# Optimization experiments

Measured on AMD Instinct MI355X. Metric: run time of the kernel, lower is better.

The kernel has to match this reference:

```python
import jax, jax.numpy as jnp
import numpy as np

V, D, N, T, U, E = 200000, 128, 50000, 20, 128, 128

def setup_inputs() -> dict:
    key = jax.random.key(0)
    ks = jax.random.split(key, 12)
    s = 0.02
    return {
        "node_ids": jax.random.randint(ks[0], (N,), 0, V, dtype=jnp.int32),
        "neigh_ids": jax.random.randint(ks[1], (N, T), 0, V, dtype=jnp.int32),
        "alpha": jax.random.uniform(ks[2], (N, T), dtype=jnp.float32),
        "table": jax.random.normal(ks[3], (V, D), dtype=jnp.float32),
        "Wq": jax.random.normal(ks[4], (D, U), dtype=jnp.float32) * s,
        "bq": jnp.zeros((U,), dtype=jnp.float32),
        "Wn": jax.random.normal(ks[5], (D, U), dtype=jnp.float32) * s,
        "bn": jnp.zeros((U,), dtype=jnp.float32),
        "Ww": jax.random.normal(ks[6], (2 * U, U), dtype=jnp.float32) * s,
        "bw": jnp.zeros((U,), dtype=jnp.float32),
        "Wg": jax.random.normal(ks[7], (U, E), dtype=jnp.float32) * s,
        "bg": jnp.zeros((E,), dtype=jnp.float32),
    }

def reference(node_ids, neigh_ids, alpha, table, Wq, bq, Wn, bn, Ww, bw, Wg, bg):
    # gather initial embeddings (irregular indexing)
    node_x = table[node_ids]            # [N, D]
    neigh_x = table[neigh_ids]          # [N, T, D]
    # Convolve: node branch Dense+ReLU
    node_h = jax.nn.relu(node_x @ Wq + bq)                       # [N, U]
    # Aggregator: neighbor Dense+ReLU then alpha-weighted matmul
    neigh_h = jax.nn.relu(jnp.einsum('ntd,du->ntu', neigh_x, Wn) + bn)  # [N, T, U]
    agg = jnp.einsum('nt,ntu->nu', alpha, neigh_h)               # [N, U]
    # concat + Dense+ReLU
    emb = jax.nn.relu(jnp.concatenate([node_h, agg], axis=-1) @ Ww + bw)  # [N, U]
    # global (Frobenius) L2 normalize, as in tf.divide(Emb, tf.norm(Emb, ord=2))
    emb = emb / jnp.linalg.norm(emb)
    # final Dense+ReLU to emb_dim
    return jax.nn.relu(emb @ Wg + bg)                            # [N, E]
```

## Files before the change

kernel.cpp:

```cpp
#include <hip/hip_runtime.h>
#include <math.h>


using f32x4  = __attribute__((ext_vector_type(4))) float;
using short8 = __attribute__((ext_vector_type(8))) short;

__device__ __forceinline__ ushort f2bf(float f) {
    uint u = __float_as_uint(f);
    return (ushort)((u + 0x7fffu + ((u >> 16) & 1u)) >> 16);
}
__device__ __forceinline__ float bf2f(ushort h) {
    return __uint_as_float((uint)h << 16);
}
__device__ __forceinline__ uint pk2(float lo, float hi) {
    return (uint)f2bf(lo) | ((uint)f2bf(hi) << 16);
}
__device__ __forceinline__ short8 pack8(f32x4 a, f32x4 b) {
    uint u0 = pk2(a[0], a[1]), u1 = pk2(a[2], a[3]);
    uint u2 = pk2(b[0], b[1]), u3 = pk2(b[2], b[3]);
    uint4 r; r.x = u0; r.y = u1; r.z = u2; r.w = u3;
    union { uint4 u; short8 s; } cv; cv.u = r; return cv.s;
}

__global__ __launch_bounds__(256)
void prep_weights(const float* __restrict__ Wq, const float* __restrict__ Wn,
                  const float* __restrict__ Ww, const float* __restrict__ Wg,
                  ushort* __restrict__ WqT, ushort* __restrict__ WnT,
                  ushort* __restrict__ WwT, ushort* __restrict__ WgT)
{
    int idx = blockIdx.x * 256 + threadIdx.x;
    const float* W; ushort* WT; int K; int j = idx;
    if (j < 16384)      { W = Wq; WT = WqT; K = 128; }
    else if (j < 32768) { W = Wn; WT = WnT; K = 128; j -= 16384; }
    else if (j < 65536) { W = Ww; WT = WwT; K = 256; j -= 32768; }
    else                { W = Wg; WT = WgT; K = 128; j -= 65536; }
    int n = j & 127, k = j >> 7;
    WT[(size_t)n * K + k] = f2bf(W[j]);
}

template<int KTOT, bool GATHER, bool AFP32, bool SUMSQ, bool SCALE, bool OUTFP32>
__global__ __launch_bounds__(256, 2)
void mfma_gemm(const void* __restrict__ Av, int lda,
               const int* __restrict__ gidx,
               const ushort* __restrict__ WT,
               const float* __restrict__ bias,
               void* __restrict__ outv, int ldo, int M,
               float* __restrict__ partials,
               const float* __restrict__ scale_ptr)
{
    __shared__ __align__(16) ushort Blds[128 * 128];
    __shared__ float red[256];

    const int tid = threadIdx.x;
    const int w = tid >> 6, l = tid & 63;
    const int l16 = l & 15, lh = l >> 4;
    const int brow = blockIdx.x * 128;

    const int row0 = brow + 32 * w + l16;
    const int row1 = row0 + 16;
    int g0 = (row0 < M) ? row0 : (M - 1);
    int g1 = (row1 < M) ? row1 : (M - 1);
    if (GATHER) { g0 = gidx[g0]; g1 = gidx[g1]; }

    f32x4 acc[2][8];
#pragma unroll
    for (int nt = 0; nt < 2; ++nt)
#pragma unroll
        for (int mt = 0; mt < 8; ++mt)
#pragma unroll
            for (int i = 0; i < 4; ++i) acc[nt][mt][i] = 0.f;

    for (int kc = 0; kc < KTOT / 128; ++kc) {
        const int kbase = kc * 128;

        short8 a[2][4];
        f32x4 t[2][8];
        if (AFP32) {
            const float* A = (const float*)Av;
#pragma unroll
            for (int nt = 0; nt < 2; ++nt) {
                const float* rp = A + (size_t)(nt ? g1 : g0) * lda + kbase + 8 * lh;
#pragma unroll
                for (int ks = 0; ks < 4; ++ks) {
                    t[nt][2 * ks]     = *reinterpret_cast<const f32x4*>(rp + 32 * ks);
                    t[nt][2 * ks + 1] = *reinterpret_cast<const f32x4*>(rp + 32 * ks + 4);
                }
            }
        } else {
            const ushort* A = (const ushort*)Av;
#pragma unroll
            for (int nt = 0; nt < 2; ++nt) {
                const ushort* rp = A + (size_t)(nt ? g1 : g0) * lda + kbase + 8 * lh;
#pragma unroll
                for (int ks = 0; ks < 4; ++ks)
                    a[nt][ks] = *reinterpret_cast<const short8*>(rp + 32 * ks);
            }
        }

        if (kc > 0) __syncthreads();
#pragma unroll
        for (int it = 0; it < 8; ++it) {
            int idx = it * 256 + tid;
            int n = idx >> 4, o = idx & 15;
            uint4 v = *reinterpret_cast<const uint4*>(&WT[(size_t)n * KTOT + kbase + 8 * o]);
            *reinterpret_cast<uint4*>(
                (char*)Blds + n * 256 + ((16 * o) ^ ((n & 7) << 4))) = v;
        }
        __syncthreads();

        if (AFP32) {
#pragma unroll
            for (int nt = 0; nt < 2; ++nt)
#pragma unroll
                for (int ks = 0; ks < 4; ++ks)
                    a[nt][ks] = pack8(t[nt][2 * ks], t[nt][2 * ks + 1]);
        }

#pragma unroll
        for (int ks = 0; ks < 4; ++ks) {
#pragma unroll
            for (int mt = 0; mt < 8; ++mt) {
                short8 wf = *reinterpret_cast<const short8*>(
                    (char*)Blds + (16 * mt + l16) * 256 +
                    ((64 * ks + 16 * lh) ^ ((l16 & 7) << 4)));
                acc[0][mt] = __builtin_amdgcn_mfma_f32_16x16x32_bf16(wf, a[0][ks], acc[0][mt], 0, 0, 0);
                acc[1][mt] = __builtin_amdgcn_mfma_f32_16x16x32_bf16(wf, a[1][ks], acc[1][mt], 0, 0, 0);
            }
        }
    }

    const float scale = SCALE ? scale_ptr[0] : 1.0f;
    float ssq = 0.f;
#pragma unroll
    for (int nt = 0; nt < 2; ++nt) {
        const int row = nt ? row1 : row0;
        const bool ok = row < M;
#pragma unroll
        for (int mt = 0; mt < 8; ++mt) {
            const f32x4 bv = *reinterpret_cast<const f32x4*>(&bias[16 * mt + 4 * lh]);
            f32x4 v;
#pragma unroll
            for (int i = 0; i < 4; ++i)
                v[i] = fmaxf(fmaf(acc[nt][mt][i], scale, bv[i]), 0.f);
            if (SUMSQ && ok)
                ssq += v[0] * v[0] + v[1] * v[1] + v[2] * v[2] + v[3] * v[3];
            if (OUTFP32) {
                if (ok)
                    *reinterpret_cast<f32x4*>(
                        &((float*)outv)[(size_t)row * ldo + 16 * mt + 4 * lh]) = v;
            } else {
                uint2 p; p.x = pk2(v[0], v[1]); p.y = pk2(v[2], v[3]);
                if (ok)
                    *reinterpret_cast<uint2*>(
                        &((ushort*)outv)[(size_t)row * ldo + 16 * mt + 4 * lh]) = p;
            }
        }
    }

    if (SUMSQ) {
        red[tid] = ssq;
        __syncthreads();
        for (int st = 128; st > 0; st >>= 1) {
            if (tid < st) red[tid] += red[tid + st];
            __syncthreads();
        }
        if (tid == 0) partials[blockIdx.x] = red[0];
    }
}

__global__ __launch_bounds__(256)
void agg_bf16(const ushort* __restrict__ H,
              const int* __restrict__ nids,
              const float* __restrict__ alpha,
              ushort* __restrict__ outb,
              int N)
{
    const int n   = blockIdx.x * 16 + (threadIdx.x >> 4);
    const int l16 = threadIdx.x & 15;
    if (n >= N) return;

    const int*   idp = &nids[n * 20];
    const float* alp = &alpha[n * 20];
    float a[8];
#pragma unroll
    for (int j = 0; j < 8; ++j) a[j] = 0.f;

#pragma unroll
    for (int t = 0; t < 20; ++t) {
        const int   id = idp[t];
        const float al = alp[t];
        uint4 h = *reinterpret_cast<const uint4*>(&H[(size_t)id * 128 + 8 * l16]);
        a[0] = fmaf(al, bf2f((ushort)(h.x & 0xffff)), a[0]);
        a[1] = fmaf(al, bf2f((ushort)(h.x >> 16)),    a[1]);
        a[2] = fmaf(al, bf2f((ushort)(h.y & 0xffff)), a[2]);
        a[3] = fmaf(al, bf2f((ushort)(h.y >> 16)),    a[3]);
        a[4] = fmaf(al, bf2f((ushort)(h.z & 0xffff)), a[4]);
        a[5] = fmaf(al, bf2f((ushort)(h.z >> 16)),    a[5]);
        a[6] = fmaf(al, bf2f((ushort)(h.w & 0xffff)), a[6]);
        a[7] = fmaf(al, bf2f((ushort)(h.w >> 16)),    a[7]);
    }
    uint4 p;
    p.x = pk2(a[0], a[1]);
    p.y = pk2(a[2], a[3]);
    p.z = pk2(a[4], a[5]);
    p.w = pk2(a[6], a[7]);
    *reinterpret_cast<uint4*>(&outb[(size_t)n * 256 + 8 * l16]) = p;
}

__global__ void reduce_norm(const float* __restrict__ partials, int n,
                            float* __restrict__ scale)
{
    __shared__ float red[256];
    float s = 0.f;
    for (int i = threadIdx.x; i < n; i += 256) s += partials[i];
    red[threadIdx.x] = s;
    __syncthreads();
    for (int st = 128; st > 0; st >>= 1) {
        if (threadIdx.x < st) red[threadIdx.x] += red[threadIdx.x + st];
        __syncthreads();
    }
    if (threadIdx.x == 0) scale[0] = 1.0f / sqrtf(red[0]);
}

extern "C" void kernel_launch(void* const* d_in, const int* in_sizes, int n_in,
                              void* d_out, int out_size, void* d_ws, size_t ws_size,
                              hipStream_t stream)
{
    const int*   node_ids  = (const int*)  d_in[0];
    const int*   neigh_ids = (const int*)  d_in[1];
    const float* alpha     = (const float*)d_in[2];
    const float* table     = (const float*)d_in[3];
    const float* Wq        = (const float*)d_in[4];
    const float* bq        = (const float*)d_in[5];
    const float* Wn        = (const float*)d_in[6];
    const float* bn        = (const float*)d_in[7];
    const float* Ww        = (const float*)d_in[8];
    const float* bw        = (const float*)d_in[9];
    const float* Wg        = (const float*)d_in[10];
    const float* bg        = (const float*)d_in[11];

    const int N = in_sizes[0];
    const int V = in_sizes[3] / 128;
    float* out = (float*)d_out;

    ushort* H    = (ushort*)d_ws;
    ushort* nh   = H    + (size_t)V * 128;
    ushort* embb = nh   + (size_t)N * 256;
    ushort* WqT  = embb + (size_t)N * 128;
    ushort* WnT  = WqT  + 16384;
    ushort* WwT  = WnT  + 16384;
    ushort* WgT  = WwT  + 32768;
    float*  partials = (float*)(WgT + 16384);
    float*  scale    = partials + 512;

    const size_t need = (size_t)((char*)(scale + 16) - (char*)d_ws);
    if (ws_size < need) return;

    const int nblkN = (N + 127) / 128;
    const int nblkV = (V + 127) / 128;

    prep_weights<<<320, 256, 0, stream>>>(Wq, Wn, Ww, Wg, WqT, WnT, WwT, WgT);
    mfma_gemm<128, false, true, false, false, false><<<nblkV, 256, 0, stream>>>(
        table, 128, nullptr, WnT, bn, H, 128, V, nullptr, nullptr);
    mfma_gemm<128, true, true, false, false, false><<<nblkN, 256, 0, stream>>>(
        table, 128, node_ids, WqT, bq, nh, 256, N, nullptr, nullptr);
    agg_bf16<<<(N + 15) / 16, 256, 0, stream>>>(H, neigh_ids, alpha, nh + 128, N);
    mfma_gemm<256, false, false, true, false, false><<<nblkN, 256, 0, stream>>>(
        nh, 256, nullptr, WwT, bw, embb, 128, N, partials, nullptr);
    reduce_norm<<<1, 256, 0, stream>>>(partials, nblkN, scale);
    mfma_gemm<128, false, false, false, true, true><<<nblkN, 256, 0, stream>>>(
        embb, 128, nullptr, WgT, bg, out, 128, N, nullptr, scale);
}
```

Baseline: 125.1 us.

## Use persistent grid-stride MFMA kernels, merge node/table GEMMs, fuse norm reduction

Replaces the generic one-shot GEMM kernel with persistent grid-stride kernels that stage weights into LDS once per block and then loop over 16-row tiles. The table-wide and gathered node GEMMs are merged into one launch that splits blocks between them, and the next tile's fp32 rows are prefetched while the current tile is computed. The norm reduction is folded into the final GEMM, which removes one launch. The aim is to amortise weight staging, cut launch count and improve latency hiding. The trade-offs are a smaller per-wave tile (16 rows instead of 32), so each weight fragment read from LDS feeds half as many MFMAs, and redundant partial-sum reduction in every final block.

```diff
diff --git a/kernel.cpp b/kernel.cpp
--- a/kernel.cpp
+++ b/kernel.cpp
@@ -16,9 +16,9 @@
     return (uint)f2bf(lo) | ((uint)f2bf(hi) << 16);
 }
 __device__ __forceinline__ short8 pack8(f32x4 a, f32x4 b) {
-    uint u0 = pk2(a[0], a[1]), u1 = pk2(a[2], a[3]);
-    uint u2 = pk2(b[0], b[1]), u3 = pk2(b[2], b[3]);
-    uint4 r; r.x = u0; r.y = u1; r.z = u2; r.w = u3;
+    uint4 r;
+    r.x = pk2(a[0], a[1]); r.y = pk2(a[2], a[3]);
+    r.z = pk2(b[0], b[1]); r.w = pk2(b[2], b[3]);
     union { uint4 u; short8 s; } cv; cv.u = r; return cv.s;
 }
 
@@ -38,133 +38,109 @@
     WT[(size_t)n * K + k] = f2bf(W[j]);
 }
 
-template<int KTOT, bool GATHER, bool AFP32, bool SUMSQ, bool SCALE, bool OUTFP32>
-__global__ __launch_bounds__(256, 2)
-void mfma_gemm(const void* __restrict__ Av, int lda,
-               const int* __restrict__ gidx,
-               const ushort* __restrict__ WT,
-               const float* __restrict__ bias,
-               void* __restrict__ outv, int ldo, int M,
-               float* __restrict__ partials,
-               const float* __restrict__ scale_ptr)
-{
-    __shared__ __align__(16) ushort Blds[128 * 128];
-    __shared__ float red[256];
-
+__device__ __forceinline__ void stage_w128(const ushort* __restrict__ WT,
+                                           const float* __restrict__ bias,
+                                           ushort* Wlds, float* blds, int tid)
+{
+#pragma unroll
+    for (int it = 0; it < 8; ++it) {
+        int idx = it * 256 + tid, n = idx >> 4, o = idx & 15;
+        uint4 v = *reinterpret_cast<const uint4*>(&WT[(size_t)n * 128 + 8 * o]);
+        *reinterpret_cast<uint4*>((char*)Wlds + n * 256 + ((16 * o) ^ ((n & 7) << 4))) = v;
+    }
+    if (tid < 128) blds[tid] = bias[tid];
+}
+
+template<bool GATHER>
+__device__ __forceinline__ void k1_loop(const float* __restrict__ table,
+                                        const int* __restrict__ gidx,
+                                        const ushort* Wlds, const float* blds,
+                                        ushort* __restrict__ out, int ldo, int M,
+                                        int wslot, int stride, int l16, int lh)
+{
+    const int nt = (M + 15) >> 4;
+    int tile = wslot;
+    if (tile >= nt) return;
+
+    f32x4 t[8];
+    {
+        int row = tile * 16 + l16; int g = (row < M) ? row : (M - 1);
+        if (GATHER) g = gidx[g];
+        const float* rp = table + (size_t)g * 128 + 8 * lh;
+#pragma unroll
+        for (int ks = 0; ks < 4; ++ks) {
+            t[2 * ks]     = *reinterpret_cast<const f32x4*>(rp + 32 * ks);
+            t[2 * ks + 1] = *reinterpret_cast<const f32x4*>(rp + 32 * ks + 4);
+        }
+    }
+    for (; tile < nt; tile += stride) {
+        short8 a[4];
+#pragma unroll
+        for (int ks = 0; ks < 4; ++ks) a[ks] = pack8(t[2 * ks], t[2 * ks + 1]);
+
+        const int nxt = tile + stride;
+        if (nxt < nt) {
+            int row = nxt * 16 + l16; int g = (row < M) ? row : (M - 1);
+            if (GATHER) g = gidx[g];
+            const float* rp = table + (size_t)g * 128 + 8 * lh;
+#pragma unroll
+            for (int ks = 0; ks < 4; ++ks) {
+                t[2 * ks]     = *reinterpret_cast<const f32x4*>(rp + 32 * ks);
+                t[2 * ks + 1] = *reinterpret_cast<const f32x4*>(rp + 32 * ks + 4);
+            }
+        }
+
+        f32x4 acc[8];
+#pragma unroll
+        for (int mt = 0; mt < 8; ++mt)
+#pragma unroll
+            for (int i = 0; i < 4; ++i) acc[mt][i] = 0.f;
+#pragma unroll
+        for (int ks = 0; ks < 4; ++ks)
+#pragma unroll
+            for (int mt = 0; mt < 8; ++mt) {
+                short8 wf = *reinterpret_cast<const short8*>(
+                    (const char*)Wlds + (16 * mt + l16) * 256 +
+                    ((64 * ks + 16 * lh) ^ ((l16 & 7) << 4)));
+                acc[mt] = __builtin_amdgcn_mfma_f32_16x16x32_bf16(wf, a[ks], acc[mt], 0, 0, 0);
+            }
+
+        const int row = tile * 16 + l16;
+        if (row < M) {
+#pragma unroll
+            for (int mt = 0; mt < 8; ++mt) {
+                f32x4 bv = *reinterpret_cast<const f32x4*>(&blds[16 * mt + 4 * lh]);
+                uint2 p;
+                p.x = pk2(fmaxf(acc[mt][0] + bv[0], 0.f), fmaxf(acc[mt][1] + bv[1], 0.f));
+                p.y = pk2(fmaxf(acc[mt][2] + bv[2], 0.f), fmaxf(acc[mt][3] + bv[3], 0.f));
+                *reinterpret_cast<uint2*>(&out[(size_t)row * ldo + 16 * mt + 4 * lh]) = p;
+            }
+        }
+    }
+}
+
+__global__ __launch_bounds__(256, 4)
+void k1_dual(const float* __restrict__ table, const int* __restrict__ node_ids,
+             const ushort* __restrict__ WnT, const float* __restrict__ bn,
+             const ushort* __restrict__ WqT, const float* __restrict__ bq,
+             ushort* __restrict__ H, ushort* __restrict__ nh,
+             int V, int N, int splitH)
+{
+    __shared__ __align__(16) ushort Wlds[128 * 128];
+    __shared__ __align__(16) float blds[128];
     const int tid = threadIdx.x;
-    const int w = tid >> 6, l = tid & 63;
-    const int l16 = l & 15, lh = l >> 4;
-    const int brow = blockIdx.x * 128;
-
-    const int row0 = brow + 32 * w + l16;
-    const int row1 = row0 + 16;
-    int g0 = (row0 < M) ? row0 : (M - 1);
-    int g1 = (row1 < M) ? row1 : (M - 1);
-    if (GATHER) { g0 = gidx[g0]; g1 = gidx[g1]; }
-
-    f32x4 acc[2][8];
-#pragma unroll
-    for (int nt = 0; nt < 2; ++nt)
-#pragma unroll
-        for (int mt = 0; mt < 8; ++mt)
-#pragma unroll
-            for (int i = 0; i < 4; ++i) acc[nt][mt][i] = 0.f;
-
-    for (int kc = 0; kc < KTOT / 128; ++kc) {
-        const int kbase = kc * 128;
-
-        short8 a[2][4];
-        f32x4 t[2][8];
-        if (AFP32) {
-            const float* A = (const float*)Av;
-#pragma unroll
-            for (int nt = 0; nt < 2; ++nt) {
-                const float* rp = A + (size_t)(nt ? g1 : g0) * lda + kbase + 8 * lh;
-#pragma unroll
-                for (int ks = 0; ks < 4; ++ks) {
-                    t[nt][2 * ks]     = *reinterpret_cast<const f32x4*>(rp + 32 * ks);
-                    t[nt][2 * ks + 1] = *reinterpret_cast<const f32x4*>(rp + 32 * ks + 4);
-                }
-            }
-        } else {
-            const ushort* A = (const ushort*)Av;
-#pragma unroll
-            for (int nt = 0; nt < 2; ++nt) {
-                const ushort* rp = A + (size_t)(nt ? g1 : g0) * lda + kbase + 8 * lh;
-#pragma unroll
-                for (int ks = 0; ks < 4; ++ks)
-                    a[nt][ks] = *reinterpret_cast<const short8*>(rp + 32 * ks);
-            }
-        }
-
-        if (kc > 0) __syncthreads();
-#pragma unroll
-        for (int it = 0; it < 8; ++it) {
-            int idx = it * 256 + tid;
-            int n = idx >> 4, o = idx & 15;
-            uint4 v = *reinterpret_cast<const uint4*>(&WT[(size_t)n * KTOT + kbase + 8 * o]);
-            *reinterpret_cast<uint4*>(
-                (char*)Blds + n * 256 + ((16 * o) ^ ((n & 7) << 4))) = v;
-        }
-        __syncthreads();
-
-        if (AFP32) {
-#pragma unroll
-            for (int nt = 0; nt < 2; ++nt)
-#pragma unroll
-                for (int ks = 0; ks < 4; ++ks)
-                    a[nt][ks] = pack8(t[nt][2 * ks], t[nt][2 * ks + 1]);
-        }
-
-#pragma unroll
-        for (int ks = 0; ks < 4; ++ks) {
-#pragma unroll
-            for (int mt = 0; mt < 8; ++mt) {
-                short8 wf = *reinterpret_cast<const short8*>(
-                    (char*)Blds + (16 * mt + l16) * 256 +
-                    ((64 * ks + 16 * lh) ^ ((l16 & 7) << 4)));
-                acc[0][mt] = __builtin_amdgcn_mfma_f32_16x16x32_bf16(wf, a[0][ks], acc[0][mt], 0, 0, 0);
-                acc[1][mt] = __builtin_amdgcn_mfma_f32_16x16x32_bf16(wf, a[1][ks], acc[1][mt], 0, 0, 0);
-            }
-        }
-    }
-
-    const float scale = SCALE ? scale_ptr[0] : 1.0f;
-    float ssq = 0.f;
-#pragma unroll
-    for (int nt = 0; nt < 2; ++nt) {
-        const int row = nt ? row1 : row0;
-        const bool ok = row < M;
-#pragma unroll
-        for (int mt = 0; mt < 8; ++mt) {
-            const f32x4 bv = *reinterpret_cast<const f32x4*>(&bias[16 * mt + 4 * lh]);
-            f32x4 v;
-#pragma unroll
-            for (int i = 0; i < 4; ++i)
-                v[i] = fmaxf(fmaf(acc[nt][mt][i], scale, bv[i]), 0.f);
-            if (SUMSQ && ok)
-                ssq += v[0] * v[0] + v[1] * v[1] + v[2] * v[2] + v[3] * v[3];
-            if (OUTFP32) {
-                if (ok)
-                    *reinterpret_cast<f32x4*>(
-                        &((float*)outv)[(size_t)row * ldo + 16 * mt + 4 * lh]) = v;
-            } else {
-                uint2 p; p.x = pk2(v[0], v[1]); p.y = pk2(v[2], v[3]);
-                if (ok)
-                    *reinterpret_cast<uint2*>(
-                        &((ushort*)outv)[(size_t)row * ldo + 16 * mt + 4 * lh]) = p;
-            }
-        }
-    }
-
-    if (SUMSQ) {
-        red[tid] = ssq;
-        __syncthreads();
-        for (int st = 128; st > 0; st >>= 1) {
-            if (tid < st) red[tid] += red[tid + st];
-            __syncthreads();
-        }
-        if (tid == 0) partials[blockIdx.x] = red[0];
+    const bool isH = (int)blockIdx.x < splitH;
+
+    stage_w128(isH ? WnT : WqT, isH ? bn : bq, Wlds, blds, tid);
+    __syncthreads();
+
+    const int w = tid >> 6, l = tid & 63, l16 = l & 15, lh = l >> 4;
+    if (isH) {
+        k1_loop<false>(table, nullptr, Wlds, blds, H, 128, V,
+                       blockIdx.x * 4 + w, splitH * 4, l16, lh);
+    } else {
+        k1_loop<true>(table, node_ids, Wlds, blds, nh, 256, N,
+                      (blockIdx.x - splitH) * 4 + w, (gridDim.x - splitH) * 4, l16, lh);
     }
 }
 
@@ -184,7 +160,6 @@
     float a[8];
 #pragma unroll
     for (int j = 0; j < 8; ++j) a[j] = 0.f;
-
 #pragma unroll
     for (int t = 0; t < 20; ++t) {
         const int   id = idp[t];
@@ -200,26 +175,145 @@
         a[7] = fmaf(al, bf2f((ushort)(h.w >> 16)),    a[7]);
     }
     uint4 p;
-    p.x = pk2(a[0], a[1]);
-    p.y = pk2(a[2], a[3]);
-    p.z = pk2(a[4], a[5]);
-    p.w = pk2(a[6], a[7]);
+    p.x = pk2(a[0], a[1]); p.y = pk2(a[2], a[3]);
+    p.z = pk2(a[4], a[5]); p.w = pk2(a[6], a[7]);
     *reinterpret_cast<uint4*>(&outb[(size_t)n * 256 + 8 * l16]) = p;
 }
 
-__global__ void reduce_norm(const float* __restrict__ partials, int n,
-                            float* __restrict__ scale)
-{
+__global__ __launch_bounds__(256, 2)
+void k3_emb(const ushort* __restrict__ nh, const ushort* __restrict__ WwT,
+            const float* __restrict__ bw, ushort* __restrict__ embb,
+            float* __restrict__ partials, int N)
+{
+    __shared__ __align__(16) ushort Wlds[128 * 256];
+    __shared__ __align__(16) float blds[128];
     __shared__ float red[256];
+    const int tid = threadIdx.x;
+#pragma unroll
+    for (int it = 0; it < 16; ++it) {
+        int idx = it * 256 + tid, n = idx >> 5, o = idx & 31;
+        uint4 v = *reinterpret_cast<const uint4*>(&WwT[(size_t)n * 256 + 8 * o]);
+        *reinterpret_cast<uint4*>((char*)Wlds + n * 512 + ((16 * o) ^ ((n & 7) << 4))) = v;
+    }
+    if (tid < 128) blds[tid] = bw[tid];
+    __syncthreads();
+
+    const int w = tid >> 6, l = tid & 63, l16 = l & 15, lh = l >> 4;
+    const int nt = (N + 15) >> 4, stride = gridDim.x * 4;
+    float ssq = 0.f;
+
+    for (int tile = blockIdx.x * 4 + w; tile < nt; tile += stride) {
+        const int row = tile * 16 + l16;
+        const int g = (row < N) ? row : (N - 1);
+        const ushort* rp = nh + (size_t)g * 256 + 8 * lh;
+        short8 a[8];
+#pragma unroll
+        for (int ks = 0; ks < 8; ++ks)
+            a[ks] = *reinterpret_cast<const short8*>(rp + 32 * ks);
+
+        f32x4 acc[8];
+#pragma unroll
+        for (int mt = 0; mt < 8; ++mt)
+#pragma unroll
+            for (int i = 0; i < 4; ++i) acc[mt][i] = 0.f;
+#pragma unroll
+        for (int ks = 0; ks < 8; ++ks)
+#pragma unroll
+            for (int mt = 0; mt < 8; ++mt) {
+                short8 wf = *reinterpret_cast<const short8*>(
+                    (const char*)Wlds + (16 * mt + l16) * 512 +
+                    ((64 * ks + 16 * lh) ^ ((l16 & 7) << 4)));
+                acc[mt] = __builtin_amdgcn_mfma_f32_16x16x32_bf16(wf, a[ks], acc[mt], 0, 0, 0);
+            }
+
+        if (row < N) {
+#pragma unroll
+            for (int mt = 0; mt < 8; ++mt) {
+                f32x4 bv = *reinterpret_cast<const f32x4*>(&blds[16 * mt + 4 * lh]);
+                f32x4 v;
+#pragma unroll
+                for (int i = 0; i < 4; ++i) {
+                    v[i] = fmaxf(acc[mt][i] + bv[i], 0.f);
+                    ssq += v[i] * v[i];
+                }
+                uint2 p; p.x = pk2(v[0], v[1]); p.y = pk2(v[2], v[3]);
+                *reinterpret_cast<uint2*>(&embb[(size_t)row * 128 + 16 * mt + 4 * lh]) = p;
+            }
+        }
+    }
+
+    red[tid] = ssq;
+    __syncthreads();
+    for (int st = 128; st > 0; st >>= 1) {
+        if (tid < st) red[tid] += red[tid + st];
+        __syncthreads();
+    }
+    if (tid == 0) partials[blockIdx.x] = red[0];
+}
+
+__global__ __launch_bounds__(256, 4)
+void k4_final(const ushort* __restrict__ embb, const ushort* __restrict__ WgT,
+              const float* __restrict__ bg, const float* __restrict__ partials,
+              int P, float* __restrict__ outp, int N)
+{
+    __shared__ __align__(16) ushort Wlds[128 * 128];
+    __shared__ __align__(16) float blds[128];
+    __shared__ float red[256];
+    __shared__ float s_scale;
+    const int tid = threadIdx.x;
+
+    stage_w128(WgT, bg, Wlds, blds, tid);
     float s = 0.f;
-    for (int i = threadIdx.x; i < n; i += 256) s += partials[i];
-    red[threadIdx.x] = s;
+    for (int i = tid; i < P; i += 256) s += partials[i];
+    red[tid] = s;
     __syncthreads();
     for (int st = 128; st > 0; st >>= 1) {
-        if (threadIdx.x < st) red[threadIdx.x] += red[threadIdx.x + st];
+        if (tid < st) red[tid] += red[tid + st];
         __syncthreads();
     }
-    if (threadIdx.x == 0) scale[0] = 1.0f / sqrtf(red[0]);
+    if (tid == 0) s_scale = 1.0f / sqrtf(red[0]);
+    __syncthreads();
+    const float scale = s_scale;
+
+    const int w = tid >> 6, l = tid & 63, l16 = l & 15, lh = l >> 4;
+    const int nt = (N + 15) >> 4, stride = gridDim.x * 4;
+
+    for (int tile = blockIdx.x * 4 + w; tile < nt; tile += stride) {
+        const int row = tile * 16 + l16;
+        const int g = (row < N) ? row : (N - 1);
+        const ushort* rp = embb + (size_t)g * 128 + 8 * lh;
+        short8 a[4];
+#pragma unroll
+        for (int ks = 0; ks < 4; ++ks)
+            a[ks] = *reinterpret_cast<const short8*>(rp + 32 * ks);
+
+        f32x4 acc[8];
+#pragma unroll
+        for (int mt = 0; mt < 8; ++mt)
+#pragma unroll
+            for (int i = 0; i < 4; ++i) acc[mt][i] = 0.f;
+#pragma unroll
+        for (int ks = 0; ks < 4; ++ks)
+#pragma unroll
+            for (int mt = 0; mt < 8; ++mt) {
+                short8 wf = *reinterpret_cast<const short8*>(
+                    (const char*)Wlds + (16 * mt + l16) * 256 +
+                    ((64 * ks + 16 * lh) ^ ((l16 & 7) << 4)));
+                acc[mt] = __builtin_amdgcn_mfma_f32_16x16x32_bf16(wf, a[ks], acc[mt], 0, 0, 0);
+            }
+
+        if (row < N) {
+#pragma unroll
+            for (int mt = 0; mt < 8; ++mt) {
+                f32x4 bv = *reinterpret_cast<const f32x4*>(&blds[16 * mt + 4 * lh]);
+                f32x4 v;
+#pragma unroll
+                for (int i = 0; i < 4; ++i)
+                    v[i] = fmaxf(fmaf(acc[mt][i], scale, bv[i]), 0.f);
+                *reinterpret_cast<f32x4*>(&outp[(size_t)row * 128 + 16 * mt + 4 * lh]) = v;
+            }
+        }
+    }
 }
 
 extern "C" void kernel_launch(void* const* d_in, const int* in_sizes, int n_in,
@@ -256,18 +350,17 @@
     const size_t need = (size_t)((char*)(scale + 16) - (char*)d_ws);
     if (ws_size < need) return;
 
-    const int nblkN = (N + 127) / 128;
-    const int nblkV = (V + 127) / 128;
+    const int G1 = 1024;
+    const long long tH = (V + 15) / 16, tN = (N + 15) / 16;
+    int splitH = (int)((G1 * tH) / (tH + tN));
+    if (splitH < 1) splitH = 1;
+    if (splitH > G1 - 1) splitH = G1 - 1;
+    const int G3 = 512, G4 = 512;
 
     prep_weights<<<320, 256, 0, stream>>>(Wq, Wn, Ww, Wg, WqT, WnT, WwT, WgT);
-    mfma_gemm<128, false, true, false, false, false><<<nblkV, 256, 0, stream>>>(
-        table, 128, nullptr, WnT, bn, H, 128, V, nullptr, nullptr);
-    mfma_gemm<128, true, true, false, false, false><<<nblkN, 256, 0, stream>>>(
-        table, 128, node_ids, WqT, bq, nh, 256, N, nullptr, nullptr);
+    k1_dual<<<G1, 256, 0, stream>>>(table, node_ids, WnT, bn, WqT, bq,
+                                    H, nh, V, N, splitH);
     agg_bf16<<<(N + 15) / 16, 256, 0, stream>>>(H, neigh_ids, alpha, nh + 128, N);
-    mfma_gemm<256, false, false, true, false, false><<<nblkN, 256, 0, stream>>>(
-        nh, 256, nullptr, WwT, bw, embb, 128, N, partials, nullptr);
-    reduce_norm<<<1, 256, 0, stream>>>(partials, nblkN, scale);
-    mfma_gemm<128, false, false, false, true, true><<<nblkN, 256, 0, stream>>>(
-        embb, 128, nullptr, WgT, bg, out, 128, N, nullptr, scale);
-}
+    k3_emb<<<G3, 256, 0, stream>>>(nh, WwT, bw, embb, partials, N);
+    k4_final<<<G4, 256, 0, stream>>>(embb, WgT, bg, partials, G3, out, N);
+}
```

Result: slower. 209.3 us (+67.3%).
